# Performance work log

Hardware: AMD Instinct MI355X
Metric: run time of the kernel (lower is better)

## Reference

```python
import jax, jax.numpy as jnp
import numpy as np

HEADS = 4
DIM_HEAD = 32
CHUNK = 1024
GROUPS = 8
EPS = 1e-5


def setup_inputs() -> dict:
    key = jax.random.key(0)
    k1, k2, k3 = jax.random.split(key, 3)
    b, dim, h, w = 8, 64, 96, 96
    inner = HEADS * DIM_HEAD  # 128
    x = jax.random.normal(k1, (b, dim, h, w), dtype=jnp.float32)
    W_qkv = jax.random.normal(k2, (3 * inner, dim), dtype=jnp.float32) * (1.0 / np.sqrt(dim))
    W_out = jax.random.normal(k3, (dim, inner), dtype=jnp.float32) * (1.0 / np.sqrt(inner))
    b_out = jnp.zeros((dim,), dtype=jnp.float32)
    gamma = jnp.ones((dim,), dtype=jnp.float32)
    beta = jnp.zeros((dim,), dtype=jnp.float32)
    return {"x": x, "W_qkv": W_qkv, "W_out": W_out, "b_out": b_out,
            "gamma": gamma, "beta": beta}


def reference(x, W_qkv, W_out, b_out, gamma, beta):
    b, c, h, w = x.shape
    n = h * w
    nch = n // CHUNK  # number of full chunks (n chosen divisible by CHUNK)
    d = DIM_HEAD
    BH = b * HEADS

    # 1x1 conv (no bias) == matmul over channel dim
    xf = x.reshape(b, c, n)
    qkv = jnp.einsum('oc,bcn->bon', W_qkv, xf)          # [b, 3*inner, n]
    q, k, v = jnp.split(qkv, 3, axis=1)                  # each [b, inner, n]

    def chunkify(t):
        # [b, inner, n] -> [BH, nch, d, CHUNK]; slicing i:i+CHUNK on last axis
        # equals reshaping n -> (nch, CHUNK) in order.
        return t.reshape(BH, d, nch, CHUNK).transpose(0, 2, 1, 3)

    qc, kc, vc = chunkify(q), chunkify(k), chunkify(v)

    qs = jax.nn.softmax(qc, axis=-1)  # softmax over chunk spatial positions
    ks = jax.nn.softmax(kc, axis=-2)  # softmax over head channels

    # context = k_chunk^T @ v_chunk : [BH, nch, CHUNK, CHUNK]
    ctx = jnp.einsum('gkdi,gkdj->gkij', ks, vc)
    # chunk_out = q_chunk @ context : [BH, nch, d, CHUNK]
    out = jnp.einsum('gkdi,gkij->gkdj', qs, ctx)

    # concat chunks back along spatial dim, reshape to image layout
    out = out.transpose(0, 2, 1, 3).reshape(b, HEADS * d, h, w)

    # to_out: 1x1 conv with bias, then GroupNorm(8, dim)
    y = jnp.einsum('oc,bchw->bohw', W_out, out) + b_out[None, :, None, None]

    yg = y.reshape(b, GROUPS, c // GROUPS, h, w)
    mu = jnp.mean(yg, axis=(2, 3, 4), keepdims=True)
    var = jnp.var(yg, axis=(2, 3, 4), keepdims=True)
    yn = ((yg - mu) * jax.lax.rsqrt(var + EPS)).reshape(b, c, h, w)
    return yn * gamma[None, :, None, None] + beta[None, :, None, None]
```

## Files before the change

kernel.cpp:

```cpp
#include <hip/hip_runtime.h>
#include <hip/hip_bf16.h>

#define N_POS 9216
#define NCHUNK 9
#define CHUNKN 1024
#define BATCH 8
#define CDIM 64
#define HEADS 4
#define GROUPS 8
#define EPS 1e-5f

#define VSEC_SZ ((size_t)BATCH * N_POS * 128)
#define VSEC_BYTES (VSEC_SZ * 2)
#define PPART_SZ ((size_t)32 * NCHUNK * 1024)
#define NPART 16

typedef __attribute__((ext_vector_type(8))) short short8;
typedef __attribute__((ext_vector_type(4))) float f32x4;

static __device__ inline unsigned pk2(float a, float b) {
    __hip_bfloat162 h2(__float2bfloat16(a), __float2bfloat16(b));
    return *reinterpret_cast<unsigned*>(&h2);
}
static __device__ inline float bf2f(short s) {
    union { unsigned u; float f; } c; c.u = ((unsigned)(unsigned short)s) << 16; return c.f;
}

__global__ __launch_bounds__(256) void qkp_kernel(const float* __restrict__ x,
        const float* __restrict__ Wqkv, float* __restrict__ Pparts) {
    int bx = blockIdx.x;
    int b  = blockIdx.y;
    int ck = bx >> 4, pt = bx & 15;
    int n0 = bx * 64;
    __shared__ __align__(16) char lraw[46080];
    __hip_bfloat16 (*xs)[72]  = (__hip_bfloat16(*)[72])lraw;
    __hip_bfloat16 (*wsm)[72] = (__hip_bfloat16(*)[72])(lraw + 9216);
    __hip_bfloat16 (*skT)[72] = (__hip_bfloat16(*)[72])lraw;
    int t = threadIdx.x, w = t >> 6, l = t & 63;
    int l15 = l & 15, quad = l >> 4;

    {
        int p = t & 63, cbase = (t >> 6) * 16;
        const float* xb = x + (size_t)b * CDIM * N_POS + n0 + p;
        #pragma unroll
        for (int j = 0; j < 16; j += 4) {
            float v0 = xb[(size_t)(cbase + j + 0) * N_POS];
            float v1 = xb[(size_t)(cbase + j + 1) * N_POS];
            float v2 = xb[(size_t)(cbase + j + 2) * N_POS];
            float v3 = xb[(size_t)(cbase + j + 3) * N_POS];
            uint2 u; u.x = pk2(v0, v1); u.y = pk2(v2, v3);
            *reinterpret_cast<uint2*>(&xs[p][cbase + j]) = u;
        }
    }
    {
        const float4* wr = (const float4*)Wqkv;
        #pragma unroll
        for (int j = 0; j < 16; ++j) {
            int f = t + j * 256;
            float4 v = wr[f];
            uint2 u; u.x = pk2(v.x, v.y); u.y = pk2(v.z, v.w);
            *reinterpret_cast<uint2*>(&wsm[f >> 4][(f & 15) * 4]) = u;
        }
    }
    __syncthreads();

    int mbase = (w >> 1) * 128;
    int nh = (w & 1) * 32;
    f32x4 acc[8][2];
    #pragma unroll
    for (int mt = 0; mt < 8; ++mt) { acc[mt][0] = (f32x4){0,0,0,0}; acc[mt][1] = (f32x4){0,0,0,0}; }
    #pragma unroll
    for (int ks = 0; ks < 2; ++ks) {
        int k0 = ks * 32 + quad * 8;
        short8 bfr[2];
        #pragma unroll
        for (int nt = 0; nt < 2; ++nt)
            bfr[nt] = *reinterpret_cast<const short8*>(&xs[nh + nt * 16 + l15][k0]);
        #pragma unroll
        for (int mt = 0; mt < 8; ++mt) {
            short8 afr = *reinterpret_cast<const short8*>(&wsm[mbase + mt * 16 + l15][k0]);
            acc[mt][0] = __builtin_amdgcn_mfma_f32_16x16x32_bf16(afr, bfr[0], acc[mt][0], 0, 0, 0);
            acc[mt][1] = __builtin_amdgcn_mfma_f32_16x16x32_bf16(afr, bfr[1], acc[mt][1], 0, 0, 0);
        }
    }
    __syncthreads();

    #pragma unroll
    for (int mt = 0; mt < 8; ++mt)
        #pragma unroll
        for (int nt = 0; nt < 2; ++nt) {
            int p = nh + nt * 16 + l15;
            #pragma unroll
            for (int r = 0; r < 4; ++r)
                skT[mbase + mt * 16 + quad * 4 + r][p] = __float2bfloat16(acc[mt][nt][r]);
        }
    __syncthreads();

    {
        int p = t & 63, h = t >> 6;
        float kr[32]; float mx = -1e30f;
        #pragma unroll
        for (int d = 0; d < 32; ++d) { kr[d] = bf2f(*(const short*)&skT[128 + h * 32 + d][p]); mx = fmaxf(mx, kr[d]); }
        float s = 0.f;
        #pragma unroll
        for (int d = 0; d < 32; ++d) { kr[d] = __expf(kr[d] - mx); s += kr[d]; }
        float is = 1.f / s;
        #pragma unroll
        for (int d = 0; d < 32; ++d) skT[128 + h * 32 + d][p] = __float2bfloat16(kr[d] * is);
        #pragma unroll
        for (int d = 0; d < 32; ++d) {
            float qv = bf2f(*(const short*)&skT[h * 32 + d][p]);
            skT[h * 32 + d][p] = __float2bfloat16(__expf(qv));
        }
    }
    __syncthreads();

    f32x4 pac[2][2];
    pac[0][0] = (f32x4){0,0,0,0}; pac[0][1] = (f32x4){0,0,0,0};
    pac[1][0] = (f32x4){0,0,0,0}; pac[1][1] = (f32x4){0,0,0,0};
    #pragma unroll
    for (int step = 0; step < 2; ++step) {
        int k0 = step * 32 + quad * 8;
        short8 bk[2];
        #pragma unroll
        for (int nt = 0; nt < 2; ++nt)
            bk[nt] = *reinterpret_cast<const short8*>(&skT[128 + w * 32 + nt * 16 + l15][k0]);
        #pragma unroll
        for (int mt = 0; mt < 2; ++mt) {
            short8 aq = *reinterpret_cast<const short8*>(&skT[w * 32 + mt * 16 + l15][k0]);
            pac[mt][0] = __builtin_amdgcn_mfma_f32_16x16x32_bf16(aq, bk[0], pac[mt][0], 0, 0, 0);
            pac[mt][1] = __builtin_amdgcn_mfma_f32_16x16x32_bf16(aq, bk[1], pac[mt][1], 0, 0, 0);
        }
    }
    float* Pp = Pparts + (size_t)pt * PPART_SZ + ((size_t)(b * 4 + w) * NCHUNK + ck) * 1024;
    #pragma unroll
    for (int mt = 0; mt < 2; ++mt)
        #pragma unroll
        for (int nt = 0; nt < 2; ++nt)
            #pragma unroll
            for (int r = 0; r < 4; ++r)
                Pp[(mt * 16 + quad * 4 + r) * 32 + nt * 16 + l15] = pac[mt][nt][r];
}

__global__ __launch_bounds__(256) void v_kernel(const float* __restrict__ x,
        const float* __restrict__ Wqkv, __hip_bfloat16* __restrict__ vsec) {
    int n0 = blockIdx.x * 128;
    int b  = blockIdx.y;
    __shared__ __align__(16) char lraw[36864];
    __hip_bfloat16 (*xs)[72]    = (__hip_bfloat16(*)[72])lraw;
    __hip_bfloat16 (*wsm)[72]   = (__hip_bfloat16(*)[72])(lraw + 18432);
    __hip_bfloat16 (*vbuf)[136] = (__hip_bfloat16(*)[136])lraw;
    int t = threadIdx.x, w = t >> 6, l = t & 63;
    int l15 = l & 15, quad = l >> 4;

    {
        int p = t & 127, cbase = (t >> 7) * 32;
        const float* xb = x + (size_t)b * CDIM * N_POS + n0 + p;
        #pragma unroll
        for (int j = 0; j < 32; j += 4) {
            float v0 = xb[(size_t)(cbase + j + 0) * N_POS];
            float v1 = xb[(size_t)(cbase + j + 1) * N_POS];
            float v2 = xb[(size_t)(cbase + j + 2) * N_POS];
            float v3 = xb[(size_t)(cbase + j + 3) * N_POS];
            uint2 u; u.x = pk2(v0, v1); u.y = pk2(v2, v3);
            *reinterpret_cast<uint2*>(&xs[p][cbase + j]) = u;
        }
    }
    {
        const float4* wr = (const float4*)(Wqkv + 256 * CDIM);
        #pragma unroll
        for (int j = 0; j < 8; ++j) {
            int f = t + j * 256;
            float4 v = wr[f];
            uint2 u; u.x = pk2(v.x, v.y); u.y = pk2(v.z, v.w);
            *reinterpret_cast<uint2*>(&wsm[f >> 4][(f & 15) * 4]) = u;
        }
    }
    __syncthreads();

    int nw = w * 32;
    f32x4 acc[8][2];
    #pragma unroll
    for (int mt = 0; mt < 8; ++mt) { acc[mt][0] = (f32x4){0,0,0,0}; acc[mt][1] = (f32x4){0,0,0,0}; }
    #pragma unroll
    for (int ks = 0; ks < 2; ++ks) {
        int k0 = ks * 32 + quad * 8;
        short8 bfr[2];
        #pragma unroll
        for (int nt = 0; nt < 2; ++nt)
            bfr[nt] = *reinterpret_cast<const short8*>(&xs[nw + nt * 16 + l15][k0]);
        #pragma unroll
        for (int mt = 0; mt < 8; ++mt) {
            short8 afr = *reinterpret_cast<const short8*>(&wsm[mt * 16 + l15][k0]);
            acc[mt][0] = __builtin_amdgcn_mfma_f32_16x16x32_bf16(afr, bfr[0], acc[mt][0], 0, 0, 0);
            acc[mt][1] = __builtin_amdgcn_mfma_f32_16x16x32_bf16(afr, bfr[1], acc[mt][1], 0, 0, 0);
        }
    }
    __syncthreads();

    #pragma unroll
    for (int mt = 0; mt < 8; ++mt)
        #pragma unroll
        for (int nt = 0; nt < 2; ++nt) {
            int p = nw + nt * 16 + l15;
            uint2 u;
            u.x = pk2(acc[mt][nt][0], acc[mt][nt][1]);
            u.y = pk2(acc[mt][nt][2], acc[mt][nt][3]);
            *reinterpret_cast<uint2*>(&vbuf[p][mt * 16 + quad * 4]) = u;
        }
    __syncthreads();

    __hip_bfloat16* outb = vsec + ((size_t)b * N_POS + n0) * 128;
    int rg = t >> 4, c0 = (t & 15) * 8;
    #pragma unroll
    for (int j = 0; j < 8; ++j) {
        int r = j * 16 + rg;
        *reinterpret_cast<uint4*>(outb + (size_t)r * 128 + c0) =
            *reinterpret_cast<const uint4*>(&vbuf[r][c0]);
    }
}

__global__ __launch_bounds__(256) void umat_kernel(const float* __restrict__ Wout,
        const float* __restrict__ Pparts, __hip_bfloat16* __restrict__ Ubf,
        float* __restrict__ stats) {
    int ck = blockIdx.x, b = blockIdx.y, h = blockIdx.z;
    int bh = b * 4 + h;
    int t = threadIdx.x;
    if (ck == 0 && h == 0 && t < 16) stats[b * 16 + t] = 0.f;
    __shared__ float Pl[32][32];
    __shared__ float iZ[32];
    size_t base4 = ((size_t)bh * NCHUNK + ck) * 256;
    {
        const float4* P0 = (const float4*)Pparts + base4 + t;
        float4 s = (float4){0.f, 0.f, 0.f, 0.f};
        #pragma unroll
        for (int j = 0; j < NPART; ++j) {
            float4 a = P0[j * (PPART_SZ / 4)];
            s.x += a.x; s.y += a.y; s.z += a.z; s.w += a.w;
        }
        ((float4*)Pl)[t] = s;
    }
    __syncthreads();
    if (t < 32) {
        float s = 0.f;
        #pragma unroll
        for (int c = 0; c < 32; ++c) s += Pl[t][c];
        iZ[t] = 1.f / s;
    }
    __syncthreads();
    int o = t & 63, wv = t >> 6;
    float wz[32];
    {
        const float4* wr = (const float4*)(Wout + (size_t)o * 128 + h * 32);
        #pragma unroll
        for (int j = 0; j < 8; ++j) {
            float4 f = wr[j];
            wz[j*4+0] = f.x * iZ[j*4+0]; wz[j*4+1] = f.y * iZ[j*4+1];
            wz[j*4+2] = f.z * iZ[j*4+2]; wz[j*4+3] = f.w * iZ[j*4+3];
        }
    }
    float ua[8];
    #pragma unroll
    for (int j = 0; j < 8; ++j) ua[j] = 0.f;
    for (int d = 0; d < 32; ++d) {
        float wd = wz[d];
        #pragma unroll
        for (int j = 0; j < 8; ++j) ua[j] += wd * Pl[d][wv * 8 + j];
    }
    uint4 up;
    up.x = pk2(ua[0], ua[1]); up.y = pk2(ua[2], ua[3]);
    up.z = pk2(ua[4], ua[5]); up.w = pk2(ua[6], ua[7]);
    __hip_bfloat16* Up = Ubf + ((size_t)(b * NCHUNK + ck) * 64 + o) * 128 + h * 32 + wv * 8;
    *reinterpret_cast<uint4*>(Up) = up;
}

__global__ __launch_bounds__(256) void y_kernel(const __hip_bfloat16* __restrict__ vsec,
        const __hip_bfloat16* __restrict__ Ubf, const float* __restrict__ bout,
        float* __restrict__ y, float* __restrict__ stats) {
    int bx = blockIdx.x;
    int b  = blockIdx.y;
    int ck = bx >> 3;
    __shared__ float gsum[8], gsq[8];
    int t = threadIdx.x, w = t >> 6, l = t & 63;
    int l15 = l & 15, quad = l >> 4;
    if (t < 8) { gsum[t] = 0.f; gsq[t] = 0.f; }
    __syncthreads();
    const __hip_bfloat16* vt = vsec + (size_t)b * N_POS * 128;
    const __hip_bfloat16* Ub = Ubf + (size_t)(b * NCHUNK + ck) * 64 * 128;
    int nbase = bx * 128 + w * 32;
    f32x4 acc[4][2];
    #pragma unroll
    for (int mt = 0; mt < 4; ++mt) { acc[mt][0] = (f32x4){0,0,0,0}; acc[mt][1] = (f32x4){0,0,0,0}; }
    #pragma unroll
    for (int ks = 0; ks < 4; ++ks) {
        int k0 = ks * 32 + quad * 8;
        short8 bf[2];
        #pragma unroll
        for (int nt = 0; nt < 2; ++nt)
            bf[nt] = *reinterpret_cast<const short8*>(vt + (size_t)(nbase + nt * 16 + l15) * 128 + k0);
        #pragma unroll
        for (int mt = 0; mt < 4; ++mt) {
            short8 af = *reinterpret_cast<const short8*>(Ub + (size_t)(mt * 16 + l15) * 128 + k0);
            acc[mt][0] = __builtin_amdgcn_mfma_f32_16x16x32_bf16(af, bf[0], acc[mt][0], 0, 0, 0);
            acc[mt][1] = __builtin_amdgcn_mfma_f32_16x16x32_bf16(af, bf[1], acc[mt][1], 0, 0, 0);
        }
    }
    float gsl[4], gql[4];
    #pragma unroll
    for (int mt = 0; mt < 4; ++mt) { gsl[mt] = 0.f; gql[mt] = 0.f; }
    float* yb = y + (size_t)b * CDIM * N_POS;
    #pragma unroll
    for (int mt = 0; mt < 4; ++mt) {
        float4 bo = *reinterpret_cast<const float4*>(bout + mt * 16 + quad * 4);
        const float* bop = reinterpret_cast<const float*>(&bo);
        #pragma unroll
        for (int nt = 0; nt < 2; ++nt) {
            int n = nbase + nt * 16 + l15;
            #pragma unroll
            for (int r = 0; r < 4; ++r) {
                int o = mt * 16 + quad * 4 + r;
                float val = acc[mt][nt][r] + bop[r];
                yb[(size_t)o * N_POS + n] = val;
                gsl[mt] += val; gql[mt] += val * val;
            }
        }
    }
    #pragma unroll
    for (int off = 16; off >= 1; off >>= 1) {
        #pragma unroll
        for (int mt = 0; mt < 4; ++mt) {
            gsl[mt] += __shfl_xor(gsl[mt], off, 64);
            gql[mt] += __shfl_xor(gql[mt], off, 64);
        }
    }
    if (l == 0 || l == 32) {
        int qh = quad >> 1;
        #pragma unroll
        for (int mt = 0; mt < 4; ++mt) {
            atomicAdd(&gsum[2 * mt + qh], gsl[mt]);
            atomicAdd(&gsq[2 * mt + qh], gql[mt]);
        }
    }
    __syncthreads();
    if (t < 8) {
        atomicAdd(&stats[(b * 8 + t) * 2],     gsum[t]);
        atomicAdd(&stats[(b * 8 + t) * 2 + 1], gsq[t]);
    }
}

__global__ __launch_bounds__(256) void gn_kernel(float* __restrict__ y,
        const float* __restrict__ stats, const float* __restrict__ gamma,
        const float* __restrict__ beta) {
    int i4 = blockIdx.x * 256 + threadIdx.x;
    if (i4 >= (BATCH * CDIM * N_POS) / 4) return;
    int base = i4 * 4;
    int bc = base / N_POS;
    int c = bc & 63, b = bc >> 6;
    int g = c >> 3;
    float s = stats[(b * 8 + g) * 2], q = stats[(b * 8 + g) * 2 + 1];
    const float invN = 1.f / (8.f * N_POS);
    float mean = s * invN;
    float var = q * invN - mean * mean;
    float sc = rsqrtf(var + EPS);
    float ga = gamma[c] * sc;
    float be = beta[c] - mean * sc * gamma[c];
    float4 v = ((float4*)y)[i4];
    v.x = v.x * ga + be; v.y = v.y * ga + be; v.z = v.z * ga + be; v.w = v.w * ga + be;
    ((float4*)y)[i4] = v;
}

extern "C" void kernel_launch(void* const* d_in, const int* in_sizes, int n_in,
                              void* d_out, int out_size, void* d_ws, size_t ws_size,
                              hipStream_t stream) {
    const float* x     = (const float*)d_in[0];
    const float* Wqkv  = (const float*)d_in[1];
    const float* Wout  = (const float*)d_in[2];
    const float* bout  = (const float*)d_in[3];
    const float* gamma = (const float*)d_in[4];
    const float* beta  = (const float*)d_in[5];
    float* out = (float*)d_out;

    __hip_bfloat16* vsec = (__hip_bfloat16*)d_ws;
    float* stats  = (float*)((char*)d_ws + VSEC_BYTES);
    float* Pparts = stats + 128;
    __hip_bfloat16* Ubf = (__hip_bfloat16*)(Pparts + NPART * PPART_SZ);

    qkp_kernel<<<dim3(144, BATCH), 256, 0, stream>>>(x, Wqkv, Pparts);
    v_kernel<<<dim3(72, BATCH), 256, 0, stream>>>(x, Wqkv, vsec);
    umat_kernel<<<dim3(NCHUNK, BATCH, HEADS), 256, 0, stream>>>(Wout, Pparts, Ubf, stats);
    y_kernel<<<dim3(72, BATCH), 256, 0, stream>>>(vsec, Ubf, bout, out, stats);
    gn_kernel<<<dim3((BATCH * CDIM * N_POS / 4 + 255) / 256), 256, 0, stream>>>(out, stats, gamma, beta);
}
```

Before: 127.9 us.

## Fuse V projection into QK kernel and load weight fragments from global

Merges the separate V-projection kernel into the Q/K projection kernel so x is read from global memory once per tile and one launch is removed. Each wave now also computes a slice of V (its 32 channels across all 64 positions) and writes it to vsec through an LDS staging buffer. The staged bf16 weight copy in LDS is dropped; each wave instead loads its weight fragments straight from global memory and converts them in registers. LDS per block grows to about 62 KB, which may lower occupancy, and the redundant global weight reads depend on cache hits.

```diff
diff --git a/kernel.cpp b/kernel.cpp
--- a/kernel.cpp
+++ b/kernel.cpp
@@ -3,11 +3,9 @@
 
 #define N_POS 9216
 #define NCHUNK 9
-#define CHUNKN 1024
 #define BATCH 8
 #define CDIM 64
 #define HEADS 4
-#define GROUPS 8
 #define EPS 1e-5f
 
 #define VSEC_SZ ((size_t)BATCH * N_POS * 128)
@@ -25,17 +23,26 @@
 static __device__ inline float bf2f(short s) {
     union { unsigned u; float f; } c; c.u = ((unsigned)(unsigned short)s) << 16; return c.f;
 }
-
-__global__ __launch_bounds__(256) void qkp_kernel(const float* __restrict__ x,
-        const float* __restrict__ Wqkv, float* __restrict__ Pparts) {
+static __device__ inline short8 load_wfrag(const float* __restrict__ W, int row, int k0) {
+    const float4* p = (const float4*)(W + (size_t)row * CDIM + k0);
+    float4 a = p[0], b = p[1];
+    union { short8 s; unsigned u[4]; } c;
+    c.u[0] = pk2(a.x, a.y); c.u[1] = pk2(a.z, a.w);
+    c.u[2] = pk2(b.x, b.y); c.u[3] = pk2(b.z, b.w);
+    return c.s;
+}
+
+__global__ __launch_bounds__(256) void qkvp_kernel(const float* __restrict__ x,
+        const float* __restrict__ Wqkv, __hip_bfloat16* __restrict__ vsec,
+        float* __restrict__ Pparts) {
     int bx = blockIdx.x;
     int b  = blockIdx.y;
     int ck = bx >> 4, pt = bx & 15;
     int n0 = bx * 64;
-    __shared__ __align__(16) char lraw[46080];
-    __hip_bfloat16 (*xs)[72]  = (__hip_bfloat16(*)[72])lraw;
-    __hip_bfloat16 (*wsm)[72] = (__hip_bfloat16(*)[72])(lraw + 9216);
-    __hip_bfloat16 (*skT)[72] = (__hip_bfloat16(*)[72])lraw;
+    __shared__ __align__(16) char lraw[63488];
+    __hip_bfloat16 (*skT)[72]   = (__hip_bfloat16(*)[72])lraw;
+    __hip_bfloat16 (*vbuf)[136] = (__hip_bfloat16(*)[136])(lraw + 36864);
+    __hip_bfloat16 (*xs)[72]    = (__hip_bfloat16(*)[72])(lraw + 54272);
     int t = threadIdx.x, w = t >> 6, l = t & 63;
     int l15 = l & 15, quad = l >> 4;
 
@@ -52,47 +59,59 @@
             *reinterpret_cast<uint2*>(&xs[p][cbase + j]) = u;
         }
     }
-    {
-        const float4* wr = (const float4*)Wqkv;
-        #pragma unroll
-        for (int j = 0; j < 16; ++j) {
-            int f = t + j * 256;
-            float4 v = wr[f];
-            uint2 u; u.x = pk2(v.x, v.y); u.y = pk2(v.z, v.w);
-            *reinterpret_cast<uint2*>(&wsm[f >> 4][(f & 15) * 4]) = u;
-        }
-    }
     __syncthreads();
 
     int mbase = (w >> 1) * 128;
-    int nh = (w & 1) * 32;
-    f32x4 acc[8][2];
-    #pragma unroll
-    for (int mt = 0; mt < 8; ++mt) { acc[mt][0] = (f32x4){0,0,0,0}; acc[mt][1] = (f32x4){0,0,0,0}; }
+    int nsel = (w & 1) * 2;
+    f32x4 qacc[8][2];
+    f32x4 vacc[2][4];
+    #pragma unroll
+    for (int mt = 0; mt < 8; ++mt) { qacc[mt][0] = (f32x4){0,0,0,0}; qacc[mt][1] = (f32x4){0,0,0,0}; }
+    #pragma unroll
+    for (int mt = 0; mt < 2; ++mt)
+        #pragma unroll
+        for (int nt = 0; nt < 4; ++nt) vacc[mt][nt] = (f32x4){0,0,0,0};
+
     #pragma unroll
     for (int ks = 0; ks < 2; ++ks) {
         int k0 = ks * 32 + quad * 8;
-        short8 bfr[2];
-        #pragma unroll
-        for (int nt = 0; nt < 2; ++nt)
-            bfr[nt] = *reinterpret_cast<const short8*>(&xs[nh + nt * 16 + l15][k0]);
+        short8 bv[4];
+        #pragma unroll
+        for (int nt = 0; nt < 4; ++nt)
+            bv[nt] = *reinterpret_cast<const short8*>(&xs[nt * 16 + l15][k0]);
         #pragma unroll
         for (int mt = 0; mt < 8; ++mt) {
-            short8 afr = *reinterpret_cast<const short8*>(&wsm[mbase + mt * 16 + l15][k0]);
-            acc[mt][0] = __builtin_amdgcn_mfma_f32_16x16x32_bf16(afr, bfr[0], acc[mt][0], 0, 0, 0);
-            acc[mt][1] = __builtin_amdgcn_mfma_f32_16x16x32_bf16(afr, bfr[1], acc[mt][1], 0, 0, 0);
-        }
-    }
-    __syncthreads();
+            short8 afr = load_wfrag(Wqkv, mbase + mt * 16 + l15, k0);
+            qacc[mt][0] = __builtin_amdgcn_mfma_f32_16x16x32_bf16(afr, bv[nsel + 0], qacc[mt][0], 0, 0, 0);
+            qacc[mt][1] = __builtin_amdgcn_mfma_f32_16x16x32_bf16(afr, bv[nsel + 1], qacc[mt][1], 0, 0, 0);
+        }
+        #pragma unroll
+        for (int mt = 0; mt < 2; ++mt) {
+            short8 afr = load_wfrag(Wqkv, 256 + (2 * w + mt) * 16 + l15, k0);
+            #pragma unroll
+            for (int nt = 0; nt < 4; ++nt)
+                vacc[mt][nt] = __builtin_amdgcn_mfma_f32_16x16x32_bf16(afr, bv[nt], vacc[mt][nt], 0, 0, 0);
+        }
+    }
 
     #pragma unroll
     for (int mt = 0; mt < 8; ++mt)
         #pragma unroll
         for (int nt = 0; nt < 2; ++nt) {
-            int p = nh + nt * 16 + l15;
+            int p = nsel * 16 + nt * 16 + l15;
             #pragma unroll
             for (int r = 0; r < 4; ++r)
-                skT[mbase + mt * 16 + quad * 4 + r][p] = __float2bfloat16(acc[mt][nt][r]);
+                skT[mbase + mt * 16 + quad * 4 + r][p] = __float2bfloat16(qacc[mt][nt][r]);
+        }
+    #pragma unroll
+    for (int mt = 0; mt < 2; ++mt)
+        #pragma unroll
+        for (int nt = 0; nt < 4; ++nt) {
+            int p = nt * 16 + l15;
+            uint2 u;
+            u.x = pk2(vacc[mt][nt][0], vacc[mt][nt][1]);
+            u.y = pk2(vacc[mt][nt][2], vacc[mt][nt][3]);
+            *reinterpret_cast<uint2*>(&vbuf[p][(2 * w + mt) * 16 + quad * 4]) = u;
         }
     __syncthreads();
 
@@ -111,6 +130,16 @@
         for (int d = 0; d < 32; ++d) {
             float qv = bf2f(*(const short*)&skT[h * 32 + d][p]);
             skT[h * 32 + d][p] = __float2bfloat16(__expf(qv));
+        }
+    }
+    {
+        __hip_bfloat16* outb = vsec + ((size_t)b * N_POS + n0) * 128;
+        int rg = t >> 4, c0 = (t & 15) * 8;
+        #pragma unroll
+        for (int j = 0; j < 4; ++j) {
+            int r = j * 16 + rg;
+            *reinterpret_cast<uint4*>(outb + (size_t)r * 128 + c0) =
+                *reinterpret_cast<const uint4*>(&vbuf[r][c0]);
         }
     }
     __syncthreads();
@@ -140,84 +169,6 @@
             #pragma unroll
             for (int r = 0; r < 4; ++r)
                 Pp[(mt * 16 + quad * 4 + r) * 32 + nt * 16 + l15] = pac[mt][nt][r];
-}
-
-__global__ __launch_bounds__(256) void v_kernel(const float* __restrict__ x,
-        const float* __restrict__ Wqkv, __hip_bfloat16* __restrict__ vsec) {
-    int n0 = blockIdx.x * 128;
-    int b  = blockIdx.y;
-    __shared__ __align__(16) char lraw[36864];
-    __hip_bfloat16 (*xs)[72]    = (__hip_bfloat16(*)[72])lraw;
-    __hip_bfloat16 (*wsm)[72]   = (__hip_bfloat16(*)[72])(lraw + 18432);
-    __hip_bfloat16 (*vbuf)[136] = (__hip_bfloat16(*)[136])lraw;
-    int t = threadIdx.x, w = t >> 6, l = t & 63;
-    int l15 = l & 15, quad = l >> 4;
-
-    {
-        int p = t & 127, cbase = (t >> 7) * 32;
-        const float* xb = x + (size_t)b * CDIM * N_POS + n0 + p;
-        #pragma unroll
-        for (int j = 0; j < 32; j += 4) {
-            float v0 = xb[(size_t)(cbase + j + 0) * N_POS];
-            float v1 = xb[(size_t)(cbase + j + 1) * N_POS];
-            float v2 = xb[(size_t)(cbase + j + 2) * N_POS];
-            float v3 = xb[(size_t)(cbase + j + 3) * N_POS];
-            uint2 u; u.x = pk2(v0, v1); u.y = pk2(v2, v3);
-            *reinterpret_cast<uint2*>(&xs[p][cbase + j]) = u;
-        }
-    }
-    {
-        const float4* wr = (const float4*)(Wqkv + 256 * CDIM);
-        #pragma unroll
-        for (int j = 0; j < 8; ++j) {
-            int f = t + j * 256;
-            float4 v = wr[f];
-            uint2 u; u.x = pk2(v.x, v.y); u.y = pk2(v.z, v.w);
-            *reinterpret_cast<uint2*>(&wsm[f >> 4][(f & 15) * 4]) = u;
-        }
-    }
-    __syncthreads();
-
-    int nw = w * 32;
-    f32x4 acc[8][2];
-    #pragma unroll
-    for (int mt = 0; mt < 8; ++mt) { acc[mt][0] = (f32x4){0,0,0,0}; acc[mt][1] = (f32x4){0,0,0,0}; }
-    #pragma unroll
-    for (int ks = 0; ks < 2; ++ks) {
-        int k0 = ks * 32 + quad * 8;
-        short8 bfr[2];
-        #pragma unroll
-        for (int nt = 0; nt < 2; ++nt)
-            bfr[nt] = *reinterpret_cast<const short8*>(&xs[nw + nt * 16 + l15][k0]);
-        #pragma unroll
-        for (int mt = 0; mt < 8; ++mt) {
-            short8 afr = *reinterpret_cast<const short8*>(&wsm[mt * 16 + l15][k0]);
-            acc[mt][0] = __builtin_amdgcn_mfma_f32_16x16x32_bf16(afr, bfr[0], acc[mt][0], 0, 0, 0);
-            acc[mt][1] = __builtin_amdgcn_mfma_f32_16x16x32_bf16(afr, bfr[1], acc[mt][1], 0, 0, 0);
-        }
-    }
-    __syncthreads();
-
-    #pragma unroll
-    for (int mt = 0; mt < 8; ++mt)
-        #pragma unroll
-        for (int nt = 0; nt < 2; ++nt) {
-            int p = nw + nt * 16 + l15;
-            uint2 u;
-            u.x = pk2(acc[mt][nt][0], acc[mt][nt][1]);
-            u.y = pk2(acc[mt][nt][2], acc[mt][nt][3]);
-            *reinterpret_cast<uint2*>(&vbuf[p][mt * 16 + quad * 4]) = u;
-        }
-    __syncthreads();
-
-    __hip_bfloat16* outb = vsec + ((size_t)b * N_POS + n0) * 128;
-    int rg = t >> 4, c0 = (t & 15) * 8;
-    #pragma unroll
-    for (int j = 0; j < 8; ++j) {
-        int r = j * 16 + rg;
-        *reinterpret_cast<uint4*>(outb + (size_t)r * 128 + c0) =
-            *reinterpret_cast<const uint4*>(&vbuf[r][c0]);
-    }
 }
 
 __global__ __launch_bounds__(256) void umat_kernel(const float* __restrict__ Wout,
@@ -385,8 +336,7 @@
     float* Pparts = stats + 128;
     __hip_bfloat16* Ubf = (__hip_bfloat16*)(Pparts + NPART * PPART_SZ);
 
-    qkp_kernel<<<dim3(144, BATCH), 256, 0, stream>>>(x, Wqkv, Pparts);
-    v_kernel<<<dim3(72, BATCH), 256, 0, stream>>>(x, Wqkv, vsec);
+    qkvp_kernel<<<dim3(144, BATCH), 256, 0, stream>>>(x, Wqkv, vsec, Pparts);
     umat_kernel<<<dim3(NCHUNK, BATCH, HEADS), 256, 0, stream>>>(Wout, Pparts, Ubf, stats);
     y_kernel<<<dim3(72, BATCH), 256, 0, stream>>>(vsec, Ubf, bout, out, stats);
     gn_kernel<<<dim3((BATCH * CDIM * N_POS / 4 + 255) / 256), 256, 0, stream>>>(out, stats, gamma, beta);
```

Measured after the change: 145.4 us. +13.7%, slower.
